# Optimization experiments

Measured on AMD Instinct MI355X. Metric: run time of the kernel, lower is better.

## Reference

```python
import jax, jax.numpy as jnp
import numpy as np

N_NODES = 100000
N_EDGES = 3200000
IN_CH = 128
HID = 16


def setup_inputs() -> dict:
    key = jax.random.key(0)
    ks = jax.random.split(key, 6)
    x = jax.random.normal(ks[0], (N_NODES, IN_CH), dtype=jnp.float32)
    edge_index = jax.random.randint(ks[1], (2, N_EDGES), 0, N_NODES, dtype=jnp.int32)
    W1 = jax.random.normal(ks[2], (IN_CH, HID), dtype=jnp.float32) / np.sqrt(IN_CH)
    b1 = jnp.zeros((HID,), jnp.float32)
    W2 = jax.random.normal(ks[3], (HID, HID), dtype=jnp.float32) / np.sqrt(HID)
    b2 = jnp.zeros((HID,), jnp.float32)
    Wl = jax.random.normal(ks[4], (HID, 1), dtype=jnp.float32) / np.sqrt(HID)
    bl = jnp.zeros((1,), jnp.float32)
    return {"x": x, "edge_index": edge_index, "W1": W1, "b1": b1,
            "W2": W2, "b2": b2, "Wl": Wl, "bl": bl}


def _gcn_conv(x, row, col, dinv, W, b, n_nodes):
    # PyG GCNConv: out[col] += d^{-1/2}[row] * d^{-1/2}[col] * (x @ W)[row]; + bias
    h = x @ W                                   # [N, C_out] small matmul
    norm = dinv[row] * dinv[col]                # [E+N] edge weights (with self-loops)
    msg = h[row] * norm[:, None]                # gather + scale
    out = jax.ops.segment_sum(msg, col, num_segments=n_nodes)  # scatter-add
    return out + b


def reference(x, edge_index, W1, b1, W2, b2, Wl, bl):
    n = x.shape[0]
    loops = jnp.arange(n, dtype=edge_index.dtype)
    row = jnp.concatenate([edge_index[0], loops])  # sources (with self-loops)
    col = jnp.concatenate([edge_index[1], loops])  # targets
    # symmetric normalization degrees computed on A + I at target index
    deg = jax.ops.segment_sum(jnp.ones(col.shape[0], x.dtype), col, num_segments=n)
    dinv = jnp.where(deg > 0, jax.lax.rsqrt(deg), 0.0)
    h = jax.nn.relu(_gcn_conv(x, row, col, dinv, W1, b1, n))
    h = jax.nn.relu(_gcn_conv(h, row, col, dinv, W2, b2, n))
    return h @ Wl + bl
```

## Files before the change

### kernel.cpp

```cpp
#include <hip/hip_runtime.h>

#define IN_CH 128
#define HID 16
#define SHIFT 8
#define BN 256
#define CAPSH 14
#define CAP (1 << CAPSH)
#define CA 16384
#define MAXNB 512

typedef int vint4 __attribute__((ext_vector_type(4)));


__global__ __launch_bounds__(1024) void scatter_kernel(
    const int* __restrict__ row, const int* __restrict__ col,
    int* __restrict__ gcur, int* __restrict__ tmp, int e, int NB) {
    __shared__ int4 ccache[CA / 4];
    __shared__ int hist[MAXNB];
    __shared__ int cur[MAXNB];
    int j = blockIdx.x, t = threadIdx.x;
    for (int b = t; b < NB; b += 1024) hist[b] = 0;
    __syncthreads();
    int e4 = e >> 2;
    const int4* c4p = (const int4*)col;
    const int4* r4p = (const int4*)row;
#pragma unroll
    for (int k = 0; k < CA / 4096; ++k) {
        int i4 = j * (CA / 4) + k * 1024 + t;
        if (i4 < e4) {
            int4 c = c4p[i4];
            ccache[k * 1024 + t] = c;
            atomicAdd(&hist[c.x >> SHIFT], 1);
            atomicAdd(&hist[c.y >> SHIFT], 1);
            atomicAdd(&hist[c.z >> SHIFT], 1);
            atomicAdd(&hist[c.w >> SHIFT], 1);
        }
    }
    if (j == gridDim.x - 1) {
        for (int i = (e & ~3) + t; i < e; i += 1024) atomicAdd(&hist[col[i] >> SHIFT], 1);
    }
    __syncthreads();
    for (int b = t; b < NB; b += 1024) {
        int h = hist[b];
        cur[b] = (b << CAPSH) + (h ? atomicAdd(&gcur[b << 4], h) : 0);
    }
    __syncthreads();
#pragma unroll
    for (int k = 0; k < CA / 4096; ++k) {
        int i4 = j * (CA / 4) + k * 1024 + t;
        if (i4 < e4) {
            int4 c = ccache[k * 1024 + t];
            int4 r = r4p[i4];
            int b0, p0;
            b0 = c.x >> SHIFT; p0 = atomicAdd(&cur[b0], 1);
            if (p0 < (b0 << CAPSH) + CAP) tmp[p0] = (r.x << SHIFT) | (c.x & (BN - 1));
            b0 = c.y >> SHIFT; p0 = atomicAdd(&cur[b0], 1);
            if (p0 < (b0 << CAPSH) + CAP) tmp[p0] = (r.y << SHIFT) | (c.y & (BN - 1));
            b0 = c.z >> SHIFT; p0 = atomicAdd(&cur[b0], 1);
            if (p0 < (b0 << CAPSH) + CAP) tmp[p0] = (r.z << SHIFT) | (c.z & (BN - 1));
            b0 = c.w >> SHIFT; p0 = atomicAdd(&cur[b0], 1);
            if (p0 < (b0 << CAPSH) + CAP) tmp[p0] = (r.w << SHIFT) | (c.w & (BN - 1));
        }
    }
    if (j == gridDim.x - 1) {
        for (int i = (e & ~3) + t; i < e; i += 1024) {
            int c = col[i], r = row[i];
            int b0 = c >> SHIFT;
            int p0 = atomicAdd(&cur[b0], 1);
            if (p0 < (b0 << CAPSH) + CAP) tmp[p0] = (r << SHIFT) | (c & (BN - 1));
        }
    }
}


__global__ __launch_bounds__(1024) void bucketCD_kernel(
    int* __restrict__ tmp, const int* __restrict__ gcur,
    int* __restrict__ row_ptr, int* __restrict__ pend,
    float* __restrict__ dinv, float* __restrict__ hs2, int n, int NB) {
    __shared__ int sbuf[CAP];
    __shared__ int hcnt[256];
    __shared__ int scn[256];
    __shared__ int cur[256];
    int b = blockIdx.x, t = threadIdx.x;
    int cnt = gcur[b << 4]; if (cnt > CAP) cnt = CAP;
    int bs = b << CAPSH;
    if (t < 256) hcnt[t] = 0;
    for (int i = t; i < cnt; i += 1024) sbuf[i] = tmp[bs + i];
    __syncthreads();
    for (int i = t; i < cnt; i += 1024) atomicAdd(&hcnt[sbuf[i] & (BN - 1)], 1);
    __syncthreads();
    int c = 0, pc = 0;
    if (t < 256) {
        c = hcnt[t];
        pc = (c + 7) & ~7;
        scn[t] = pc;
    }
    __syncthreads();
    for (int off = 1; off < 256; off <<= 1) {
        int a = (t >= off && t < 256) ? scn[t - off] : 0;
        __syncthreads();
        if (t < 256) scn[t] += a;
        __syncthreads();
    }
    int rp = 0;
    if (t < 256) {
        rp = bs + scn[t] - pc;
        int node = (b << SHIFT) + t;
        if (node < n) {
            row_ptr[node] = rp;
            pend[node] = rp + pc;
            dinv[node] = rsqrtf((float)(c + 1));
        }
        cur[t] = rp;
    }
    if (b == 0) {
        if (t == 0) dinv[n] = 0.0f;
        if (t >= 256 && t < 256 + HID) hs2[(size_t)n * HID + (t - 256)] = 0.0f;
    }
    __syncthreads();
    for (int i = t; i < cnt; i += 1024) {
        int u = sbuf[i];
        int pos = atomicAdd(&cur[u & (BN - 1)], 1);
        tmp[pos] = u >> SHIFT;
    }
    __syncthreads();
    if (t < 256) {
        int pe = rp + pc;
        for (int p = cur[t]; p < pe; ++p) tmp[p] = n;
    }
}


__global__ __launch_bounds__(256) void gemm1_kernel(
    const float* __restrict__ x, const float* __restrict__ W1,
    const float* __restrict__ dinv, float* __restrict__ hs, int n) {
    __shared__ float4 swl[512];
    int t = threadIdx.x;
#pragma unroll
    for (int i = t; i < 512; i += 256) {
        float4 v = ((const float4*)W1)[i];
        int k = i >> 2, q = i & 3;
        int kp = ((k & 31) << 2) | (k >> 5);
        swl[kp * 4 + q] = v;
    }
    __syncthreads();
    int gid = blockIdx.x * 256 + t;
    int r = gid >> 2;
    int sub = gid & 3;
    if (r > n) return;
    float4 xv[8];
    if (r < n) {
        const float4* xp = (const float4*)(x + (size_t)r * IN_CH + sub * 32);
#pragma unroll
        for (int j = 0; j < 8; ++j) xv[j] = xp[j];
    } else {
#pragma unroll
        for (int j = 0; j < 8; ++j) xv[j] = make_float4(0.f, 0.f, 0.f, 0.f);
    }
    float acc[16];
#pragma unroll
    for (int c = 0; c < 16; ++c) acc[c] = 0.f;
#pragma unroll
    for (int j = 0; j < 8; ++j) {
#pragma unroll
        for (int q = 0; q < 4; ++q) {
            int jq = j * 4 + q;
            float xs = (q == 0) ? xv[j].x : (q == 1) ? xv[j].y : (q == 2) ? xv[j].z : xv[j].w;
            const float4* wp = &swl[(jq * 4 + sub) * 4];
            float4 w0 = wp[0], w1 = wp[1], w2 = wp[2], w3 = wp[3];
            acc[0]  = fmaf(xs, w0.x, acc[0]);
            acc[1]  = fmaf(xs, w0.y, acc[1]);
            acc[2]  = fmaf(xs, w0.z, acc[2]);
            acc[3]  = fmaf(xs, w0.w, acc[3]);
            acc[4]  = fmaf(xs, w1.x, acc[4]);
            acc[5]  = fmaf(xs, w1.y, acc[5]);
            acc[6]  = fmaf(xs, w1.z, acc[6]);
            acc[7]  = fmaf(xs, w1.w, acc[7]);
            acc[8]  = fmaf(xs, w2.x, acc[8]);
            acc[9]  = fmaf(xs, w2.y, acc[9]);
            acc[10] = fmaf(xs, w2.z, acc[10]);
            acc[11] = fmaf(xs, w2.w, acc[11]);
            acc[12] = fmaf(xs, w3.x, acc[12]);
            acc[13] = fmaf(xs, w3.y, acc[13]);
            acc[14] = fmaf(xs, w3.z, acc[14]);
            acc[15] = fmaf(xs, w3.w, acc[15]);
        }
    }
#pragma unroll
    for (int c = 0; c < 16; ++c) {
        acc[c] += __shfl_xor(acc[c], 1);
        acc[c] += __shfl_xor(acc[c], 2);
    }
    float dg = (r < n) ? dinv[r] : 0.0f;
    float4 o;
    o.x = dg * acc[sub * 4 + 0];
    o.y = dg * acc[sub * 4 + 1];
    o.z = dg * acc[sub * 4 + 2];
    o.w = dg * acc[sub * 4 + 3];
    ((float4*)hs)[(size_t)r * 4 + sub] = o;
}


#define AGG_GATHER_LOOP                                                          \
    int beg = __builtin_nontemporal_load(row_ptr + node);                        \
    int end = __builtin_nontemporal_load(pend + node);                           \
    int j = beg + (qd << 3);                                                     \
    vint4 p0, p1;                                                                \
    if (j < end) {                                                               \
        p0 = __builtin_nontemporal_load((const vint4*)(pk + j));                 \
        p1 = __builtin_nontemporal_load((const vint4*)(pk + j + 4));             \
    }                                                                            \
    while (j < end) {                                                            \
        int jn = j + 16;                                                         \
        vint4 q0, q1;                                                            \
        if (jn < end) {                                                          \
            q0 = __builtin_nontemporal_load((const vint4*)(pk + jn));            \
            q1 = __builtin_nontemporal_load((const vint4*)(pk + jn + 4));        \
        }                                                                        \
        float4 v0 = h4[(size_t)p0.x * 4 + sub];                                  \
        float4 v1 = h4[(size_t)p0.y * 4 + sub];                                  \
        float4 v2 = h4[(size_t)p0.z * 4 + sub];                                  \
        float4 v3 = h4[(size_t)p0.w * 4 + sub];                                  \
        float4 v4 = h4[(size_t)p1.x * 4 + sub];                                  \
        float4 v5 = h4[(size_t)p1.y * 4 + sub];                                  \
        float4 v6 = h4[(size_t)p1.z * 4 + sub];                                  \
        float4 v7 = h4[(size_t)p1.w * 4 + sub];                                  \
        cx += ((v0.x + v1.x) + (v2.x + v3.x)) + ((v4.x + v5.x) + (v6.x + v7.x)); \
        cy += ((v0.y + v1.y) + (v2.y + v3.y)) + ((v4.y + v5.y) + (v6.y + v7.y)); \
        cz += ((v0.z + v1.z) + (v2.z + v3.z)) + ((v4.z + v5.z) + (v6.z + v7.z)); \
        cw += ((v0.w + v1.w) + (v2.w + v3.w)) + ((v4.w + v5.w) + (v6.w + v7.w)); \
        p0 = q0; p1 = q1; j = jn;                                                \
    }                                                                            \
    cx += __shfl_xor(cx, 4);                                                     \
    cy += __shfl_xor(cy, 4);                                                     \
    cz += __shfl_xor(cz, 4);                                                     \
    cw += __shfl_xor(cw, 4);

__global__ __launch_bounds__(256) void agg1_kernel(
    const float* __restrict__ hs, const int* __restrict__ row_ptr,
    const int* __restrict__ pend, const int* __restrict__ pk,
    const float* __restrict__ dinv,
    const float* __restrict__ b1, const float* __restrict__ W2,
    float* __restrict__ hs2, int n) {
    int t = threadIdx.x;
    int node = blockIdx.x * 32 + (t >> 3);
    int sub = t & 3;
    int qd  = (t >> 2) & 1;
    if (node >= n) return;
    const float4* h4 = (const float4*)hs;
    float4 self = h4[(size_t)node * 4 + sub];
    float cx = qd ? 0.f : self.x, cy = qd ? 0.f : self.y;
    float cz = qd ? 0.f : self.z, cw = qd ? 0.f : self.w;
    AGG_GATHER_LOOP
    float dg = dinv[node];
    float4 b1v = *(const float4*)(b1 + (sub << 2));
    float ax = fmaxf(fmaf(dg, cx, b1v.x), 0.f);
    float ay = fmaxf(fmaf(dg, cy, b1v.y), 0.f);
    float az = fmaxf(fmaf(dg, cz, b1v.z), 0.f);
    float aw = fmaxf(fmaf(dg, cw, b1v.w), 0.f);
    float ox = 0.f, oy = 0.f, oz = 0.f, ow = 0.f;
#pragma unroll
    for (int r = 0; r < 4; ++r) {
        float fx = __shfl_xor(ax, r);
        float fy = __shfl_xor(ay, r);
        float fz = __shfl_xor(az, r);
        float fw = __shfl_xor(aw, r);
        int kb = (sub ^ r) << 2;
        const float* wp = W2 + kb * HID + (sub << 2);
        float4 w0 = *(const float4*)(wp);
        float4 w1 = *(const float4*)(wp + HID);
        float4 w2 = *(const float4*)(wp + 2 * HID);
        float4 w3 = *(const float4*)(wp + 3 * HID);
        ox += fx * w0.x + fy * w1.x + fz * w2.x + fw * w3.x;
        oy += fx * w0.y + fy * w1.y + fz * w2.y + fw * w3.y;
        oz += fx * w0.z + fy * w1.z + fz * w2.z + fw * w3.z;
        ow += fx * w0.w + fy * w1.w + fz * w2.w + fw * w3.w;
    }
    if (qd == 0) {
        float4 o; o.x = dg * ox; o.y = dg * oy; o.z = dg * oz; o.w = dg * ow;
        ((float4*)hs2)[(size_t)node * 4 + sub] = o;
    }
}

__global__ __launch_bounds__(256) void agg2_kernel(
    const float* __restrict__ hs2, const int* __restrict__ row_ptr,
    const int* __restrict__ pend, const int* __restrict__ pk,
    const float* __restrict__ dinv,
    const float* __restrict__ b2, const float* __restrict__ Wl,
    const float* __restrict__ bl, float* __restrict__ out, int n) {
    int t = threadIdx.x;
    int node = blockIdx.x * 32 + (t >> 3);
    int sub = t & 3;
    int qd  = (t >> 2) & 1;
    if (node >= n) return;
    const float4* h4 = (const float4*)hs2;
    float4 self = h4[(size_t)node * 4 + sub];
    float cx = qd ? 0.f : self.x, cy = qd ? 0.f : self.y;
    float cz = qd ? 0.f : self.z, cw = qd ? 0.f : self.w;
    AGG_GATHER_LOOP
    float dg = dinv[node];
    float4 b2v = *(const float4*)(b2 + (sub << 2));
    float4 wlv = *(const float4*)(Wl + (sub << 2));
    float p = fmaxf(fmaf(dg, cx, b2v.x), 0.f) * wlv.x
            + fmaxf(fmaf(dg, cy, b2v.y), 0.f) * wlv.y
            + fmaxf(fmaf(dg, cz, b2v.z), 0.f) * wlv.z
            + fmaxf(fmaf(dg, cw, b2v.w), 0.f) * wlv.w;
    p += __shfl_xor(p, 1);
    p += __shfl_xor(p, 2);
    if ((t & 7) == 0) out[node] = p + bl[0];
}

extern "C" void kernel_launch(void* const* d_in, const int* in_sizes, int n_in,
                              void* d_out, int out_size, void* d_ws, size_t ws_size,
                              hipStream_t stream) {
    const float* x  = (const float*)d_in[0];
    const int*   ei = (const int*)d_in[1];
    const float* W1 = (const float*)d_in[2];
    const float* b1 = (const float*)d_in[3];
    const float* W2 = (const float*)d_in[4];
    const float* b2 = (const float*)d_in[5];
    const float* Wl = (const float*)d_in[6];
    const float* bl = (const float*)d_in[7];

    int n = in_sizes[0] / IN_CH;
    int e = in_sizes[1] / 2;
    const int* row = ei;
    const int* col = ei + e;

    int NB  = (n + BN - 1) >> SHIFT;
    int nba = (e + CA - 1) / CA;

    char* ws = (char*)d_ws;
    size_t off = 0;
    auto alloc = [&](size_t bytes) -> void* {
        void* p = ws + off;
        off = (off + bytes + 255) & ~(size_t)255;
        return p;
    };

    size_t tabf = (size_t)(n + 1) * HID;

    int*   gcur    = (int*)alloc((size_t)NB * 16 * 4);
    int*   tmp     = (int*)alloc(((size_t)NB << CAPSH) * 4);
    int*   row_ptr = (int*)alloc((size_t)n * 4);
    int*   pend    = (int*)alloc((size_t)n * 4);
    float* dinv    = (float*)alloc(((size_t)n + 1) * 4);
    float* hs      = (float*)alloc(tabf * 4);
    float* hs2     = (float*)alloc(tabf * 4);

    dim3 gG((4 * (n + 1) + 255) / 256);
    dim3 gA((8 * n + 255) / 256);

    (void)hipMemsetAsync(gcur, 0, (size_t)NB * 16 * 4, stream);
    hipLaunchKernelGGL(scatter_kernel,  dim3(nba), dim3(1024), 0, stream, row, col, gcur, tmp, e, NB);
    hipLaunchKernelGGL(bucketCD_kernel, dim3(NB),  dim3(1024), 0, stream, tmp, gcur, row_ptr, pend, dinv, hs2, n, NB);

    hipLaunchKernelGGL(gemm1_kernel, gG, dim3(256), 0, stream, x, W1, dinv, hs, n);
    hipLaunchKernelGGL(agg1_kernel,  gA, dim3(256), 0, stream, hs, row_ptr, pend, tmp, dinv, b1, W2, hs2, n);
    hipLaunchKernelGGL(agg2_kernel,  gA, dim3(256), 0, stream, hs2, row_ptr, pend, tmp, dinv, b2, Wl, bl, (float*)d_out, n);
}
```

Measured before the change: 139.8 us.

## Sort nodes by degree within each bucket to balance aggregation warps

The bucket kernel now builds a per-bucket permutation of nodes, ordered by descending padded degree using an O(256) rank count per thread. Both aggregation kernels read their node from this permutation, so nodes sharing a wavefront have similar neighbour counts and less lane divergence in the gather loop. The cost is an extra indirection load per node, a 256-iteration shared-memory loop per thread in the bucket kernel, and worse locality for the per-node output writes. Padded slots (-1 degree) sort last and exit early.

```diff
diff --git a/kernel.cpp b/kernel.cpp
--- a/kernel.cpp
+++ b/kernel.cpp
@@ -76,11 +76,13 @@
 __global__ __launch_bounds__(1024) void bucketCD_kernel(
     int* __restrict__ tmp, const int* __restrict__ gcur,
     int* __restrict__ row_ptr, int* __restrict__ pend,
-    float* __restrict__ dinv, float* __restrict__ hs2, int n, int NB) {
+    float* __restrict__ dinv, float* __restrict__ hs2,
+    int* __restrict__ nodeperm, int n, int NB) {
     __shared__ int sbuf[CAP];
     __shared__ int hcnt[256];
     __shared__ int scn[256];
     __shared__ int cur[256];
+    __shared__ int pcs[256];
     int b = blockIdx.x, t = threadIdx.x;
     int cnt = gcur[b << 4]; if (cnt > CAP) cnt = CAP;
     int bs = b << CAPSH;
@@ -90,10 +92,12 @@
     for (int i = t; i < cnt; i += 1024) atomicAdd(&hcnt[sbuf[i] & (BN - 1)], 1);
     __syncthreads();
     int c = 0, pc = 0;
+    int node = (b << SHIFT) + t;
     if (t < 256) {
         c = hcnt[t];
         pc = (c + 7) & ~7;
         scn[t] = pc;
+        pcs[t] = (node < n) ? pc : -1;
     }
     __syncthreads();
     for (int off = 1; off < 256; off <<= 1) {
@@ -105,13 +109,19 @@
     int rp = 0;
     if (t < 256) {
         rp = bs + scn[t] - pc;
-        int node = (b << SHIFT) + t;
         if (node < n) {
             row_ptr[node] = rp;
             pend[node] = rp + pc;
             dinv[node] = rsqrtf((float)(c + 1));
         }
         cur[t] = rp;
+        int my = pcs[t];
+        int rank = 0;
+        for (int jj = 0; jj < 256; ++jj) {
+            int pj = pcs[jj];
+            rank += (pj > my) || (pj == my && jj < t);
+        }
+        nodeperm[(b << SHIFT) + rank] = node;
     }
     if (b == 0) {
         if (t == 0) dinv[n] = 0.0f;
@@ -239,11 +249,12 @@
 __global__ __launch_bounds__(256) void agg1_kernel(
     const float* __restrict__ hs, const int* __restrict__ row_ptr,
     const int* __restrict__ pend, const int* __restrict__ pk,
-    const float* __restrict__ dinv,
+    const int* __restrict__ nodeperm, const float* __restrict__ dinv,
     const float* __restrict__ b1, const float* __restrict__ W2,
     float* __restrict__ hs2, int n) {
     int t = threadIdx.x;
-    int node = blockIdx.x * 32 + (t >> 3);
+    int slot = blockIdx.x * 32 + (t >> 3);
+    int node = nodeperm[slot];
     int sub = t & 3;
     int qd  = (t >> 2) & 1;
     if (node >= n) return;
@@ -285,11 +296,12 @@
 __global__ __launch_bounds__(256) void agg2_kernel(
     const float* __restrict__ hs2, const int* __restrict__ row_ptr,
     const int* __restrict__ pend, const int* __restrict__ pk,
-    const float* __restrict__ dinv,
+    const int* __restrict__ nodeperm, const float* __restrict__ dinv,
     const float* __restrict__ b2, const float* __restrict__ Wl,
     const float* __restrict__ bl, float* __restrict__ out, int n) {
     int t = threadIdx.x;
-    int node = blockIdx.x * 32 + (t >> 3);
+    int slot = blockIdx.x * 32 + (t >> 3);
+    int node = nodeperm[slot];
     int sub = t & 3;
     int qd  = (t >> 2) & 1;
     if (node >= n) return;
@@ -340,22 +352,23 @@
 
     size_t tabf = (size_t)(n + 1) * HID;
 
-    int*   gcur    = (int*)alloc((size_t)NB * 16 * 4);
-    int*   tmp     = (int*)alloc(((size_t)NB << CAPSH) * 4);
-    int*   row_ptr = (int*)alloc((size_t)n * 4);
-    int*   pend    = (int*)alloc((size_t)n * 4);
-    float* dinv    = (float*)alloc(((size_t)n + 1) * 4);
-    float* hs      = (float*)alloc(tabf * 4);
-    float* hs2     = (float*)alloc(tabf * 4);
+    int*   gcur     = (int*)alloc((size_t)NB * 16 * 4);
+    int*   tmp      = (int*)alloc(((size_t)NB << CAPSH) * 4);
+    int*   row_ptr  = (int*)alloc((size_t)n * 4);
+    int*   pend     = (int*)alloc((size_t)n * 4);
+    int*   nodeperm = (int*)alloc((size_t)NB * BN * 4);
+    float* dinv     = (float*)alloc(((size_t)n + 1) * 4);
+    float* hs       = (float*)alloc(tabf * 4);
+    float* hs2      = (float*)alloc(tabf * 4);
 
     dim3 gG((4 * (n + 1) + 255) / 256);
-    dim3 gA((8 * n + 255) / 256);
+    dim3 gA(NB * 8);
 
     (void)hipMemsetAsync(gcur, 0, (size_t)NB * 16 * 4, stream);
     hipLaunchKernelGGL(scatter_kernel,  dim3(nba), dim3(1024), 0, stream, row, col, gcur, tmp, e, NB);
-    hipLaunchKernelGGL(bucketCD_kernel, dim3(NB),  dim3(1024), 0, stream, tmp, gcur, row_ptr, pend, dinv, hs2, n, NB);
+    hipLaunchKernelGGL(bucketCD_kernel, dim3(NB),  dim3(1024), 0, stream, tmp, gcur, row_ptr, pend, dinv, hs2, nodeperm, n, NB);
 
     hipLaunchKernelGGL(gemm1_kernel, gG, dim3(256), 0, stream, x, W1, dinv, hs, n);
-    hipLaunchKernelGGL(agg1_kernel,  gA, dim3(256), 0, stream, hs, row_ptr, pend, tmp, dinv, b1, W2, hs2, n);
-    hipLaunchKernelGGL(agg2_kernel,  gA, dim3(256), 0, stream, hs2, row_ptr, pend, tmp, dinv, b2, Wl, bl, (float*)d_out, n);
-}
+    hipLaunchKernelGGL(agg1_kernel,  gA, dim3(256), 0, stream, hs, row_ptr, pend, tmp, nodeperm, dinv, b1, W2, hs2, n);
+    hipLaunchKernelGGL(agg2_kernel,  gA, dim3(256), 0, stream, hs2, row_ptr, pend, tmp, nodeperm, dinv, b2, Wl, bl, (float*)d_out, n);
+}
```

After: 162.6 us. 1.16x slower.
